# Kernel optimization log

Measured on AMD Instinct MI355X. Metric: run time of the kernel, lower is better.

## Reference

```python
import jax, jax.numpy as jnp
import numpy as np

B, S, H = 4, 2048, 576
NH, NKV, HD = 9, 3, 64
GROUPS = NH // NKV
ROPE_THETA = 100000.0
MAX_POS = 8192


def _rope_tables():
    inv_freq = 1.0 / (ROPE_THETA ** (jnp.arange(0, HD, 2, dtype=jnp.float32) / HD))
    t = jnp.arange(MAX_POS, dtype=jnp.float32)
    freqs = jnp.outer(t, inv_freq)              # [MAX_POS, HD//2]
    emb = jnp.concatenate([freqs, freqs], axis=-1)  # [MAX_POS, HD]
    return jnp.cos(emb), jnp.sin(emb)


def _rotate_half(x):
    x1, x2 = x[..., : HD // 2], x[..., HD // 2 :]
    return jnp.concatenate([-x2, x1], axis=-1)


def setup_inputs() -> dict:
    key = jax.random.key(0)
    k1, k2, k3, k4, k5 = jax.random.split(key, 5)
    hidden_states = jax.random.normal(k1, (B, S, H), dtype=jnp.float32)
    # causal additive mask [B,1,S,S]: 0 where allowed, large negative above diagonal
    causal = jnp.triu(jnp.ones((S, S), dtype=bool), k=1)
    attention_mask = jnp.where(causal, jnp.float32(-1e9), jnp.float32(0.0))[None, None]
    attention_mask = jnp.broadcast_to(attention_mask, (B, 1, S, S))
    position_ids = jnp.broadcast_to(jnp.arange(S, dtype=jnp.int32)[None, :], (B, S))
    scale = 1.0 / np.sqrt(H)
    Wq = jax.random.normal(k2, (NH * HD, H), dtype=jnp.float32) * scale
    Wk = jax.random.normal(k3, (NKV * HD, H), dtype=jnp.float32) * scale
    Wv = jax.random.normal(k4, (NKV * HD, H), dtype=jnp.float32) * scale
    Wo = jax.random.normal(k5, (H, NH * HD), dtype=jnp.float32) * scale
    return {"hidden_states": hidden_states, "attention_mask": attention_mask,
            "position_ids": position_ids, "Wq": Wq, "Wk": Wk, "Wv": Wv, "Wo": Wo}


def reference(hidden_states, attention_mask, position_ids, Wq, Wk, Wv, Wo):
    bsz, q_len, _ = hidden_states.shape
    cos_cached, sin_cached = _rope_tables()
    # projections (nn.Linear: x @ W.T), reshape to [B, heads, S, HD]
    q = (hidden_states @ Wq.T).reshape(bsz, q_len, NH, HD).transpose(0, 2, 1, 3)
    k = (hidden_states @ Wk.T).reshape(bsz, q_len, NKV, HD).transpose(0, 2, 1, 3)
    v = (hidden_states @ Wv.T).reshape(bsz, q_len, NKV, HD).transpose(0, 2, 1, 3)
    # RoPE: gather cos/sin per position, broadcast over heads
    cos = cos_cached[position_ids][:, None]  # [B,1,S,HD]
    sin = sin_cached[position_ids][:, None]
    q = q * cos + _rotate_half(q) * sin
    k = k * cos + _rotate_half(k) * sin
    # GQA: repeat_interleave kv heads
    k = jnp.repeat(k, GROUPS, axis=1)  # [B,NH,S,HD]
    v = jnp.repeat(v, GROUPS, axis=1)
    scores = jnp.einsum('bhqd,bhkd->bhqk', q, k) / np.sqrt(HD)
    scores = scores + attention_mask
    probs = jax.nn.softmax(scores.astype(jnp.float32), axis=-1).astype(q.dtype)
    attn = jnp.einsum('bhqk,bhkd->bhqd', probs, v)
    attn = attn.transpose(0, 2, 1, 3).reshape(bsz, q_len, NH * HD)
    return attn @ Wo.T
```

## Files before the change

### kernel.cpp

```cpp
#include <hip/hip_runtime.h>
#include <hip/hip_bf16.h>
#include <math.h>

#define Bsz 4
#define Slen 2048
#define Hdim 576
#define NH 9
#define NKV 3
#define HD 64

typedef __bf16 bf16_t;
typedef __bf16 bf16x8 __attribute__((ext_vector_type(8)));
typedef float f32x4 __attribute__((ext_vector_type(4)));
typedef float f32x16 __attribute__((ext_vector_type(16)));
typedef unsigned int u32;
typedef unsigned int u32x4 __attribute__((ext_vector_type(4)));

static __device__ __forceinline__ bf16x8 load_cvt8(const float* __restrict__ src){
  float4 f0 = *reinterpret_cast<const float4*>(src);
  float4 f1 = *reinterpret_cast<const float4*>(src + 4);
  bf16x8 v;
  v[0]=(bf16_t)f0.x; v[1]=(bf16_t)f0.y; v[2]=(bf16_t)f0.z; v[3]=(bf16_t)f0.w;
  v[4]=(bf16_t)f1.x; v[5]=(bf16_t)f1.y; v[6]=(bf16_t)f1.z; v[7]=(bf16_t)f1.w;
  return v;
}

static __device__ __forceinline__ void gload16(const bf16_t* g, bf16_t* l){
  __builtin_amdgcn_global_load_lds((const __attribute__((address_space(1))) void*)g,
                                   (__attribute__((address_space(3))) void*)l, 16, 0, 0);
}

__global__ void rope_table_kernel(float* __restrict__ cost, float* __restrict__ sint){
  int i = blockIdx.x * blockDim.x + threadIdx.x;
  if (i >= Slen * 32) return;
  int j = i & 31;
  int p = i >> 5;
  double invf = pow(100000.0, -(double)j / 32.0);
  double ang = (double)p * invf;
  cost[i] = (float)cos(ang);
  sint[i] = (float)sin(ang);
}

__global__ void precast_kernel(const float* __restrict__ X,
                               const float* __restrict__ Wq,
                               const float* __restrict__ Wk,
                               const float* __restrict__ Wv,
                               const float* __restrict__ Wo,
                               bf16_t* __restrict__ Xb,
                               bf16_t* __restrict__ Wb,
                               bf16_t* __restrict__ Wob)
{
  const int NX  = 8192 * 576 / 8;
  const int NWq = 576 * 576 / 8;
  const int NWk = 192 * 576 / 8;
  int i = blockIdx.x * blockDim.x + threadIdx.x;
  const int total = NX + NWq + 2 * NWk + NWq;
  if (i >= total) return;
  const float* src; bf16_t* dst; int off;
  if (i < NX)                    { src = X;  dst = Xb;            off = i; }
  else if (i < NX + NWq)         { src = Wq; dst = Wb;            off = i - NX; }
  else if (i < NX + NWq + NWk)   { src = Wk; dst = Wb + 331776;   off = i - NX - NWq; }
  else if (i < NX + NWq + 2*NWk) { src = Wv; dst = Wb + 442368;   off = i - NX - NWq - NWk; }
  else                           { src = Wo; dst = Wob;           off = i - NX - NWq - 2*NWk; }
  *reinterpret_cast<bf16x8*>(dst + (size_t)off * 8) = load_cvt8(src + (size_t)off * 8);
}

__launch_bounds__(256)
__global__ void qkv_gemm_kernel(const bf16_t* __restrict__ Xb,
                                const bf16_t* __restrict__ Wb,
                                bf16_t* __restrict__ qbuf,
                                bf16_t* __restrict__ kbuf,
                                bf16_t* __restrict__ vtbuf)
{
  __shared__ bf16_t Ald[2][128 * 64];
  __shared__ bf16_t Bld[2][64 * 64];
  const int t = threadIdx.x, l = t & 63, w = t >> 6;
  const int wm = w >> 1, wn = w & 1;
  const int lane16 = l & 15, grp = l >> 4;
  const int m0 = blockIdx.x * 128;
  const int nt = blockIdx.y;
  const int nrow0 = nt * 64;

  const int sr = l >> 3;
  const int sc = ((l & 7) ^ sr) * 8;

  f32x4 acc[4][2];
  #pragma unroll
  for (int mi = 0; mi < 4; ++mi)
    #pragma unroll
    for (int ni = 0; ni < 2; ++ni)
      acc[mi][ni] = (f32x4){0.f, 0.f, 0.f, 0.f};

  auto STAGE = [&](int kt, int buf){
    const int k0 = kt * 64;
    #pragma unroll
    for (int u = 0; u < 4; ++u)
      gload16(Xb + (size_t)(m0 + w * 32 + u * 8 + sr) * Hdim + k0 + sc,
              &Ald[buf][(w * 32 + u * 8) * 64]);
    #pragma unroll
    for (int u = 0; u < 2; ++u)
      gload16(Wb + (size_t)(nrow0 + w * 16 + u * 8 + sr) * Hdim + k0 + sc,
              &Bld[buf][(w * 16 + u * 8) * 64]);
  };

  STAGE(0, 0);
  asm volatile("s_waitcnt vmcnt(0)" ::: "memory");
  __syncthreads();

  const int sl7 = lane16 & 7;
  for (int kt = 0; kt < 9; ++kt){
    const int buf = kt & 1;
    if (kt + 1 < 9) STAGE(kt + 1, buf ^ 1);
    #pragma unroll
    for (int ks = 0; ks < 2; ++ks){
      bf16x8 a[4], bb[2];
      #pragma unroll
      for (int mi = 0; mi < 4; ++mi){
        int row = wm * 64 + mi * 16 + lane16;
        a[mi] = *reinterpret_cast<const bf16x8*>(&Ald[buf][row * 64 + (((ks * 4 + grp) ^ sl7) * 8)]);
      }
      #pragma unroll
      for (int ni = 0; ni < 2; ++ni){
        int row = wn * 32 + ni * 16 + lane16;
        bb[ni] = *reinterpret_cast<const bf16x8*>(&Bld[buf][row * 64 + (((ks * 4 + grp) ^ sl7) * 8)]);
      }
      #pragma unroll
      for (int mi = 0; mi < 4; ++mi)
        #pragma unroll
        for (int ni = 0; ni < 2; ++ni)
          acc[mi][ni] = __builtin_amdgcn_mfma_f32_16x16x32_bf16(a[mi], bb[ni], acc[mi][ni], 0, 0, 0);
    }
    if (kt + 1 < 9){
      asm volatile("s_waitcnt vmcnt(0)" ::: "memory");
      __syncthreads();
    }
  }

  #pragma unroll
  for (int mi = 0; mi < 4; ++mi){
    #pragma unroll
    for (int ni = 0; ni < 2; ++ni){
      #pragma unroll
      for (int j = 0; j < 4; ++j){
        int m = m0 + wm * 64 + mi * 16 + grp * 4 + j;
        int dl = wn * 32 + ni * 16 + lane16;
        int b = m >> 11;
        int s = m & 2047;
        bf16_t v = (bf16_t)acc[mi][ni][j];
        if (nt < 9)
          qbuf[(((size_t)b * NH + nt) * Slen + s) * HD + dl] = v;
        else if (nt < 12)
          kbuf[(((size_t)b * NKV + (nt - 9)) * Slen + s) * HD + dl] = v;
        else
          vtbuf[(((size_t)b * NKV + (nt - 12)) * HD + dl) * Slen + s] = v;
      }
    }
  }
}

__global__ void rope_apply_all(bf16_t* __restrict__ qkbuf, const int* __restrict__ pos_ids,
                               const float* __restrict__ cost, const float* __restrict__ sint,
                               float qscale)
{
  int idx = blockIdx.x * blockDim.x + threadIdx.x;
  const int qrows = Bsz * NH * Slen;
  const int total = qrows + Bsz * NKV * Slen;
  if (idx >= total) return;
  const bool isq = idx < qrows;
  int s = idx & (Slen - 1);
  int b = isq ? idx / (NH * Slen) : (idx - qrows) / (NKV * Slen);
  float scale = isq ? qscale : 1.0f;
  bf16_t* row = qkbuf + (size_t)idx * HD;
  int pos = pos_ids[b * Slen + s];
  const float* cp = cost + (size_t)pos * 32;
  const float* sp = sint + (size_t)pos * 32;
  float x[64];
  #pragma unroll
  for (int v = 0; v < 8; ++v){
    bf16x8 t8 = *reinterpret_cast<const bf16x8*>(row + v * 8);
    #pragma unroll
    for (int i = 0; i < 8; ++i) x[v * 8 + i] = (float)t8[i];
  }
  bf16_t o[64];
  #pragma unroll
  for (int j = 0; j < 32; ++j){
    float c = cp[j], sn = sp[j];
    o[j]      = (bf16_t)((x[j] * c - x[j + 32] * sn) * scale);
    o[j + 32] = (bf16_t)((x[j + 32] * c + x[j] * sn) * scale);
  }
  #pragma unroll
  for (int v = 0; v < 8; ++v)
    *reinterpret_cast<bf16x8*>(row + v * 8) = *reinterpret_cast<bf16x8*>(o + v * 8);
}

__launch_bounds__(128)
__global__ void flash_attn_kernel(const bf16_t* __restrict__ qbuf,
                                  const bf16_t* __restrict__ kbuf,
                                  const bf16_t* __restrict__ vtbuf,
                                  bf16_t* __restrict__ attn_out,
                                  u32* __restrict__ part_O,
                                  float* __restrict__ part_ml)
{
  __shared__ bf16_t Kld[2][32 * 64];
  __shared__ bf16_t Vld[2][64 * 32];
  const int t = threadIdx.x, l = t & 63, w = t >> 6;
  const int l32 = l & 31, hi = l >> 5;

  const int flat = blockIdx.x;
  const int v = flat / 36;
  const int bh = flat % 36;
  int qt, t0, t1, seg;
  if (v < 16){ qt = 16 + v; t0 = 0; t1 = 32; seg = 0; }
  else {
    int i = (v - 16) >> 1;
    if (((v - 16) & 1) == 0){ qt = 15 - i; t0 = 0; t1 = 2 * qt + 2; seg = -1; }
    else                    { qt = 31 - i; t0 = 32; t1 = 2 * qt + 2; seg = 1; }
  }
  const int b = bh / NH, h = bh % NH, kvh = h / (NH / NKV);

  const bf16_t* qp = qbuf + ((size_t)b * NH + h) * Slen * HD;
  const bf16_t* kp = kbuf + ((size_t)b * NKV + kvh) * Slen * HD;
  const bf16_t* vp = vtbuf + ((size_t)b * NKV + kvh) * HD * Slen;

  const int q0 = qt * 64 + w * 32;
  bf16x8 aq[4];
  #pragma unroll
  for (int ds = 0; ds < 4; ++ds)
    aq[ds] = *reinterpret_cast<const bf16x8*>(qp + (size_t)(q0 + l32) * HD + ds * 16 + hi * 8);

  f32x16 acco[2];
  #pragma unroll
  for (int db = 0; db < 2; ++db)
    #pragma unroll
    for (int r = 0; r < 16; ++r) acco[db][r] = 0.f;
  float mrun = -1e30f, lrun = 0.f;

  const int krow = l >> 3;
  const int ksc  = ((l & 7) ^ krow) * 8;
  const int vrow = l >> 2;
  const int vsc  = ((l & 3) ^ (vrow & 3)) * 8;

  auto STAGE = [&](int kt, int buf){
    const int k0 = kt * 32;
    #pragma unroll
    for (int u = 0; u < 2; ++u){
      int ub = w * 2 + u;
      gload16(kp + (size_t)(k0 + ub * 8 + krow) * HD + ksc, &Kld[buf][ub * 512]);
      gload16(vp + (size_t)(ub * 16 + vrow) * Slen + k0 + vsc, &Vld[buf][ub * 512]);
    }
  };

  int cur = 0;
  STAGE(t0, 0);
  asm volatile("s_waitcnt vmcnt(0)" ::: "memory");
  __syncthreads();

  const int dt = 2 * qt + w;
  for (int kb = t0; kb < t1; ++kb){
    if (kb + 1 < t1) STAGE(kb + 1, cur ^ 1);

    if (kb <= dt){
      f32x16 sacc;
      #pragma unroll
      for (int r = 0; r < 16; ++r) sacc[r] = 0.f;
      __builtin_amdgcn_s_setprio(1);
      #pragma unroll
      for (int ds = 0; ds < 4; ++ds){
        bf16x8 ak = *reinterpret_cast<const bf16x8*>(
            &Kld[cur][l32 * 64 + (((ds * 2 + hi) ^ (l32 & 7)) * 8)]);
        sacc = __builtin_amdgcn_mfma_f32_32x32x16_bf16(ak, aq[ds], sacc, 0, 0, 0);
      }
      __builtin_amdgcn_s_setprio(0);

      if (kb == dt){
        #pragma unroll
        for (int r = 0; r < 16; ++r){
          int crow = (r & 3) + 8 * (r >> 2) + 4 * hi;
          if (crow > l32) sacc[r] = -1e30f;
        }
      }

      float tmax = fmaxf(sacc[0], sacc[1]);
      #pragma unroll
      for (int r = 2; r < 16; ++r) tmax = fmaxf(tmax, sacc[r]);
      tmax = fmaxf(tmax, __shfl_xor(tmax, 32, 64));

      if (__ballot(tmax - mrun > 8.f)){
        float mnew = fmaxf(mrun, tmax);
        float sf = __builtin_amdgcn_exp2f(mrun - mnew);
        lrun *= sf;
        #pragma unroll
        for (int db = 0; db < 2; ++db)
          #pragma unroll
          for (int r = 0; r < 16; ++r) acco[db][r] *= sf;
        mrun = mnew;
      }

      float rsum = 0.f;
      #pragma unroll
      for (int r = 0; r < 16; ++r){
        float pv = __builtin_amdgcn_exp2f(sacc[r] - mrun);
        sacc[r] = pv;
        rsum += pv;
      }
      rsum += __shfl_xor(rsum, 32, 64);
      lrun += rsum;

      u32 wv[8];
      #pragma unroll
      for (int j = 0; j < 8; ++j){
        float lo = sacc[2 * j], hp = sacc[2 * j + 1];
        asm("v_cvt_pk_bf16_f32 %0, %1, %2" : "=v"(wv[j]) : "v"(lo), "v"(hp));
      }
      asm volatile("v_permlane32_swap_b32 %0, %1" : "+v"(wv[0]), "+v"(wv[2]));
      asm volatile("v_permlane32_swap_b32 %0, %1" : "+v"(wv[1]), "+v"(wv[3]));
      asm volatile("v_permlane32_swap_b32 %0, %1" : "+v"(wv[4]), "+v"(wv[6]));
      asm volatile("v_permlane32_swap_b32 %0, %1" : "+v"(wv[5]), "+v"(wv[7]));
      u32x4 pa0 = (u32x4){wv[0], wv[1], wv[2], wv[3]};
      u32x4 pa1 = (u32x4){wv[4], wv[5], wv[6], wv[7]};

      __builtin_amdgcn_s_setprio(1);
      #pragma unroll
      for (int ks = 0; ks < 2; ++ks){
        #pragma unroll
        for (int db = 0; db < 2; ++db){
          bf16x8 av = *reinterpret_cast<const bf16x8*>(
              &Vld[cur][(db * 32 + l32) * 32 + (((ks * 2 + hi) ^ (l32 & 3)) * 8)]);
          acco[db] = __builtin_amdgcn_mfma_f32_32x32x16_bf16(
              av, __builtin_bit_cast(bf16x8, ks ? pa1 : pa0), acco[db], 0, 0, 0);
        }
      }
      __builtin_amdgcn_s_setprio(0);
    }

    asm volatile("s_waitcnt vmcnt(0)" ::: "memory");
    __syncthreads();
    cur ^= 1;
  }

  if (seg < 0){
    const float linv = 1.0f / lrun;
    const int srow = q0 + l32;
    bf16_t* orow = attn_out + ((size_t)b * Slen + srow) * (NH * HD) + h * HD;
    #pragma unroll
    for (int db = 0; db < 2; ++db){
      #pragma unroll
      for (int j = 0; j < 8; ++j){
        int r = 2 * j;
        int d = db * 32 + (r & 3) + 8 * (r >> 2) + 4 * hi;
        u32 pw;
        float lo = acco[db][r] * linv, hp = acco[db][r + 1] * linv;
        asm("v_cvt_pk_bf16_f32 %0, %1, %2" : "=v"(pw) : "v"(lo), "v"(hp));
        *reinterpret_cast<u32*>(orow + d) = pw;
      }
    }
  } else {
    const int slot = (bh * 16 + (qt - 16)) * 2 + seg;
    u32* po = part_O + ((size_t)slot * 2 + w) * 1024;
    float* pml = part_ml + ((size_t)slot * 2 + w) * 64;
    #pragma unroll
    for (int db = 0; db < 2; ++db){
      #pragma unroll
      for (int j = 0; j < 8; ++j){
        int r = 2 * j;
        int d = db * 32 + (r & 3) + 8 * (r >> 2) + 4 * hi;
        u32 pw;
        float lo = acco[db][r], hp = acco[db][r + 1];
        asm("v_cvt_pk_bf16_f32 %0, %1, %2" : "=v"(pw) : "v"(lo), "v"(hp));
        po[(d >> 1) * 32 + l32] = pw;
      }
    }
    if (hi == 0){ pml[l32] = mrun; pml[32 + l32] = lrun; }
  }
}

__launch_bounds__(128)
__global__ void combine_kernel(const u32* __restrict__ part_O,
                               const float* __restrict__ part_ml,
                               bf16_t* __restrict__ attn_out)
{
  const int idx = blockIdx.x;
  const int bh = idx % 36, qtm = idx / 36;
  const int qt = 16 + qtm;
  const int b = bh / NH, h = bh % NH;
  const int t = threadIdx.x;
  const int q = t & 31, wg = (t >> 5) & 1, half = t >> 6;
  const int slot0 = (bh * 16 + qtm) * 2;

  const float* pml0 = part_ml + ((size_t)(slot0 + 0) * 2 + wg) * 64;
  const float* pml1 = part_ml + ((size_t)(slot0 + 1) * 2 + wg) * 64;
  float m1 = pml0[q], l1 = pml0[32 + q];
  float m2 = pml1[q], l2 = pml1[32 + q];
  float m = fmaxf(m1, m2);
  float a1 = __builtin_amdgcn_exp2f(m1 - m);
  float a2 = __builtin_amdgcn_exp2f(m2 - m);
  float linv = 1.0f / (l1 * a1 + l2 * a2);
  a1 *= linv; a2 *= linv;

  const u32* po0 = part_O + ((size_t)(slot0 + 0) * 2 + wg) * 1024;
  const u32* po1 = part_O + ((size_t)(slot0 + 1) * 2 + wg) * 1024;
  const int s = qt * 64 + wg * 32 + q;
  bf16_t* orow = attn_out + ((size_t)b * Slen + s) * (NH * HD) + h * HD;

  #pragma unroll
  for (int u = 0; u < 16; ++u){
    int dp = half * 16 + u;
    u32 v1 = po0[dp * 32 + q], v2 = po1[dp * 32 + q];
    float lo = a1 * __builtin_bit_cast(float, v1 << 16)
             + a2 * __builtin_bit_cast(float, v2 << 16);
    float hv = a1 * __builtin_bit_cast(float, v1 & 0xffff0000u)
             + a2 * __builtin_bit_cast(float, v2 & 0xffff0000u);
    u32 pw;
    asm("v_cvt_pk_bf16_f32 %0, %1, %2" : "=v"(pw) : "v"(lo), "v"(hv));
    *reinterpret_cast<u32*>(orow + 2 * dp) = pw;
  }
}

__launch_bounds__(256)
__global__ void out_gemm_kernel(const bf16_t* __restrict__ A,
                                const bf16_t* __restrict__ Wob,
                                float* __restrict__ out)
{
  __shared__ bf16_t Ald[2][128 * 64];
  __shared__ bf16_t Bld[2][64 * 64];
  const int t = threadIdx.x, l = t & 63, w = t >> 6;
  const int wm = w >> 1, wn = w & 1;
  const int lane16 = l & 15, grp = l >> 4;
  const int m0 = blockIdx.x * 128;
  const int nt = blockIdx.y;
  const int nrow0 = nt * 64;

  const int sr = l >> 3;
  const int sc = ((l & 7) ^ sr) * 8;

  f32x4 acc[4][2];
  #pragma unroll
  for (int mi = 0; mi < 4; ++mi)
    #pragma unroll
    for (int ni = 0; ni < 2; ++ni)
      acc[mi][ni] = (f32x4){0.f, 0.f, 0.f, 0.f};

  auto STAGE = [&](int kt, int buf){
    const int k0 = kt * 64;
    #pragma unroll
    for (int u = 0; u < 4; ++u)
      gload16(A + (size_t)(m0 + w * 32 + u * 8 + sr) * Hdim + k0 + sc,
              &Ald[buf][(w * 32 + u * 8) * 64]);
    #pragma unroll
    for (int u = 0; u < 2; ++u)
      gload16(Wob + (size_t)(nrow0 + w * 16 + u * 8 + sr) * Hdim + k0 + sc,
              &Bld[buf][(w * 16 + u * 8) * 64]);
  };

  STAGE(0, 0);
  asm volatile("s_waitcnt vmcnt(0)" ::: "memory");
  __syncthreads();

  const int sl7 = lane16 & 7;
  for (int kt = 0; kt < 9; ++kt){
    const int buf = kt & 1;
    if (kt + 1 < 9) STAGE(kt + 1, buf ^ 1);
    #pragma unroll
    for (int ks = 0; ks < 2; ++ks){
      bf16x8 a[4], bb[2];
      #pragma unroll
      for (int mi = 0; mi < 4; ++mi){
        int row = wm * 64 + mi * 16 + lane16;
        a[mi] = *reinterpret_cast<const bf16x8*>(&Ald[buf][row * 64 + (((ks * 4 + grp) ^ sl7) * 8)]);
      }
      #pragma unroll
      for (int ni = 0; ni < 2; ++ni){
        int row = wn * 32 + ni * 16 + lane16;
        bb[ni] = *reinterpret_cast<const bf16x8*>(&Bld[buf][row * 64 + (((ks * 4 + grp) ^ sl7) * 8)]);
      }
      #pragma unroll
      for (int mi = 0; mi < 4; ++mi)
        #pragma unroll
        for (int ni = 0; ni < 2; ++ni)
          acc[mi][ni] = __builtin_amdgcn_mfma_f32_16x16x32_bf16(a[mi], bb[ni], acc[mi][ni], 0, 0, 0);
    }
    if (kt + 1 < 9){
      asm volatile("s_waitcnt vmcnt(0)" ::: "memory");
      __syncthreads();
    }
  }

  #pragma unroll
  for (int mi = 0; mi < 4; ++mi){
    #pragma unroll
    for (int ni = 0; ni < 2; ++ni){
      #pragma unroll
      for (int j = 0; j < 4; ++j){
        int m = m0 + wm * 64 + mi * 16 + grp * 4 + j;
        int n = nrow0 + wn * 32 + ni * 16 + lane16;
        out[(size_t)m * Hdim + n] = acc[mi][ni][j];
      }
    }
  }
}

extern "C" void kernel_launch(void* const* d_in, const int* in_sizes, int n_in,
                              void* d_out, int out_size, void* d_ws, size_t ws_size,
                              hipStream_t stream) {
  const float* X   = (const float*)d_in[0];
  const int* pos   = (const int*)d_in[2];
  const float* Wq  = (const float*)d_in[3];
  const float* Wk  = (const float*)d_in[4];
  const float* Wv  = (const float*)d_in[5];
  const float* Wo  = (const float*)d_in[6];
  float* out = (float*)d_out;

  char* ws = (char*)d_ws;
  float* cost = (float*)ws;
  float* sint = (float*)(ws + 262144);
  bf16_t* qb  = (bf16_t*)(ws + 524288);
  bf16_t* kb  = qb + (size_t)Bsz * NH * Slen * HD;
  bf16_t* vt  = kb + (size_t)Bsz * NKV * Slen * HD;
  bf16_t* Xb  = vt + (size_t)Bsz * NKV * Slen * HD;
  bf16_t* ab  = Xb;
  bf16_t* Wb  = Xb + (size_t)8192 * 576;
  bf16_t* Wob = Wb + (size_t)960 * 576;
  u32*  part_O  = (u32*)(Wob + (size_t)576 * 576);
  float* part_ml = (float*)(part_O + (size_t)1152 * 2 * 1024);

  const float QSCALE = 0.125f * 1.44269504088896f;

  rope_table_kernel<<<dim3((Slen * 32 + 255) / 256), dim3(256), 0, stream>>>(cost, sint);
  precast_kernel<<<dim3(2736), dim3(256), 0, stream>>>(X, Wq, Wk, Wv, Wo, Xb, Wb, Wob);
  qkv_gemm_kernel<<<dim3(64, 15), dim3(256), 0, stream>>>(Xb, Wb, qb, kb, vt);
  rope_apply_all<<<dim3((Bsz * (NH + NKV) * Slen + 255) / 256), dim3(256), 0, stream>>>(qb, pos, cost, sint, QSCALE);
  flash_attn_kernel<<<dim3(1728), dim3(128), 0, stream>>>(qb, kb, vt, ab, part_O, part_ml);
  combine_kernel<<<dim3(576), dim3(128), 0, stream>>>(part_O, part_ml, ab);
  out_gemm_kernel<<<dim3(64, 9), dim3(256), 0, stream>>>(ab, Wob, out);
}
```

Before: 118.9 us.

## Triple-buffer flash attention K/V loads and merge setup kernels

The flash attention kernel moves from double to triple buffering of K/V tiles in LDS. It prefetches two tiles ahead, waits with a partial vmcnt, and issues a single barrier per iteration instead of waiting on all loads at the end. The Q loads are moved after the first stages are issued, and the V swizzle is changed to a different XOR pattern, likely to reduce bank conflicts. The rope table and precast kernels are fused into one launch to save a kernel launch. The cost is more LDS per block, which may lower occupancy.

```diff
diff --git a/kernel.cpp b/kernel.cpp
--- a/kernel.cpp
+++ b/kernel.cpp
@@ -30,30 +30,32 @@
                                    (__attribute__((address_space(3))) void*)l, 16, 0, 0);
 }
 
-__global__ void rope_table_kernel(float* __restrict__ cost, float* __restrict__ sint){
-  int i = blockIdx.x * blockDim.x + threadIdx.x;
-  if (i >= Slen * 32) return;
-  int j = i & 31;
-  int p = i >> 5;
-  double invf = pow(100000.0, -(double)j / 32.0);
-  double ang = (double)p * invf;
-  cost[i] = (float)cos(ang);
-  sint[i] = (float)sin(ang);
-}
-
-__global__ void precast_kernel(const float* __restrict__ X,
-                               const float* __restrict__ Wq,
-                               const float* __restrict__ Wk,
-                               const float* __restrict__ Wv,
-                               const float* __restrict__ Wo,
-                               bf16_t* __restrict__ Xb,
-                               bf16_t* __restrict__ Wb,
-                               bf16_t* __restrict__ Wob)
+__global__ void setup_kernel(const float* __restrict__ X,
+                             const float* __restrict__ Wq,
+                             const float* __restrict__ Wk,
+                             const float* __restrict__ Wv,
+                             const float* __restrict__ Wo,
+                             bf16_t* __restrict__ Xb,
+                             bf16_t* __restrict__ Wb,
+                             bf16_t* __restrict__ Wob,
+                             float* __restrict__ cost,
+                             float* __restrict__ sint)
 {
+  const int bid = blockIdx.x;
+  if (bid < 256){
+    int i = bid * 256 + threadIdx.x;
+    int j = i & 31;
+    int p = i >> 5;
+    double invf = pow(100000.0, -(double)j / 32.0);
+    double ang = (double)p * invf;
+    cost[i] = (float)cos(ang);
+    sint[i] = (float)sin(ang);
+    return;
+  }
   const int NX  = 8192 * 576 / 8;
   const int NWq = 576 * 576 / 8;
   const int NWk = 192 * 576 / 8;
-  int i = blockIdx.x * blockDim.x + threadIdx.x;
+  int i = (bid - 256) * 256 + threadIdx.x;
   const int total = NX + NWq + 2 * NWk + NWq;
   if (i >= total) return;
   const float* src; bf16_t* dst; int off;
@@ -201,8 +203,8 @@
                                   u32* __restrict__ part_O,
                                   float* __restrict__ part_ml)
 {
-  __shared__ bf16_t Kld[2][32 * 64];
-  __shared__ bf16_t Vld[2][64 * 32];
+  __shared__ bf16_t Kld[3][32 * 64];
+  __shared__ bf16_t Vld[3][64 * 32];
   const int t = threadIdx.x, l = t & 63, w = t >> 6;
   const int l32 = l & 31, hi = l >> 5;
 
@@ -222,23 +224,10 @@
   const bf16_t* kp = kbuf + ((size_t)b * NKV + kvh) * Slen * HD;
   const bf16_t* vp = vtbuf + ((size_t)b * NKV + kvh) * HD * Slen;
 
-  const int q0 = qt * 64 + w * 32;
-  bf16x8 aq[4];
-  #pragma unroll
-  for (int ds = 0; ds < 4; ++ds)
-    aq[ds] = *reinterpret_cast<const bf16x8*>(qp + (size_t)(q0 + l32) * HD + ds * 16 + hi * 8);
-
-  f32x16 acco[2];
-  #pragma unroll
-  for (int db = 0; db < 2; ++db)
-    #pragma unroll
-    for (int r = 0; r < 16; ++r) acco[db][r] = 0.f;
-  float mrun = -1e30f, lrun = 0.f;
-
   const int krow = l >> 3;
   const int ksc  = ((l & 7) ^ krow) * 8;
   const int vrow = l >> 2;
-  const int vsc  = ((l & 3) ^ (vrow & 3)) * 8;
+  const int vsc  = ((l & 3) ^ ((vrow >> 1) & 3)) * 8;
 
   auto STAGE = [&](int kt, int buf){
     const int k0 = kt * 32;
@@ -250,14 +239,33 @@
     }
   };
 
+  STAGE(t0, 0);
+  if (t0 + 1 < t1) STAGE(t0 + 1, 1);
+
+  const int q0 = qt * 64 + w * 32;
+  bf16x8 aq[4];
+  #pragma unroll
+  for (int ds = 0; ds < 4; ++ds)
+    aq[ds] = *reinterpret_cast<const bf16x8*>(qp + (size_t)(q0 + l32) * HD + ds * 16 + hi * 8);
+
+  f32x16 acco[2];
+  #pragma unroll
+  for (int db = 0; db < 2; ++db)
+    #pragma unroll
+    for (int r = 0; r < 16; ++r) acco[db][r] = 0.f;
+  float mrun = -1e30f, lrun = 0.f;
+
   int cur = 0;
-  STAGE(t0, 0);
-  asm volatile("s_waitcnt vmcnt(0)" ::: "memory");
-  __syncthreads();
-
   const int dt = 2 * qt + w;
   for (int kb = t0; kb < t1; ++kb){
-    if (kb + 1 < t1) STAGE(kb + 1, cur ^ 1);
+    if (kb + 1 < t1) asm volatile("s_waitcnt vmcnt(8)" ::: "memory");
+    else             asm volatile("s_waitcnt vmcnt(0)" ::: "memory");
+    __syncthreads();
+
+    if (kb + 2 < t1){
+      int sb = cur + 2; if (sb >= 3) sb -= 3;
+      STAGE(kb + 2, sb);
+    }
 
     if (kb <= dt){
       f32x16 sacc;
@@ -325,7 +333,7 @@
         #pragma unroll
         for (int db = 0; db < 2; ++db){
           bf16x8 av = *reinterpret_cast<const bf16x8*>(
-              &Vld[cur][(db * 32 + l32) * 32 + (((ks * 2 + hi) ^ (l32 & 3)) * 8)]);
+              &Vld[cur][(db * 32 + l32) * 32 + (((ks * 2 + hi) ^ ((l32 >> 1) & 3)) * 8)]);
           acco[db] = __builtin_amdgcn_mfma_f32_32x32x16_bf16(
               av, __builtin_bit_cast(bf16x8, ks ? pa1 : pa0), acco[db], 0, 0, 0);
         }
@@ -333,9 +341,7 @@
       __builtin_amdgcn_s_setprio(0);
     }
 
-    asm volatile("s_waitcnt vmcnt(0)" ::: "memory");
-    __syncthreads();
-    cur ^= 1;
+    cur = (cur + 1 == 3) ? 0 : cur + 1;
   }
 
   if (seg < 0){
@@ -525,8 +531,7 @@
 
   const float QSCALE = 0.125f * 1.44269504088896f;
 
-  rope_table_kernel<<<dim3((Slen * 32 + 255) / 256), dim3(256), 0, stream>>>(cost, sint);
-  precast_kernel<<<dim3(2736), dim3(256), 0, stream>>>(X, Wq, Wk, Wv, Wo, Xb, Wb, Wob);
+  setup_kernel<<<dim3(256 + 2736), dim3(256), 0, stream>>>(X, Wq, Wk, Wv, Wo, Xb, Wb, Wob, cost, sint);
   qkv_gemm_kernel<<<dim3(64, 15), dim3(256), 0, stream>>>(Xb, Wb, qb, kb, vt);
   rope_apply_all<<<dim3((Bsz * (NH + NKV) * Slen + 255) / 256), dim3(256), 0, stream>>>(qb, pos, cost, sint, QSCALE);
   flash_attn_kernel<<<dim3(1728), dim3(128), 0, stream>>>(qb, kb, vt, ab, part_O, part_ml);
```

Result: faster. 113.5 us (-4.6%).
